# Performance work log

Measured on AMD Instinct MI355X. Metric: run time of the kernel, lower is better.

## Reference

```python
import jax, jax.numpy as jnp
import numpy as np

NUM_CLASSES = 80
CONF_THRESH = 0.05
NMS_THRESH = 0.6
TOPK = 1000
LEVEL_HWS = [40000, 10000, 2500, 640, 160]
CLASS_OFFSET = 2.0  # > max box coordinate so different classes never overlap (class-aware NMS)


def setup_inputs() -> dict:
    key = jax.random.key(0)
    inp = {}
    for i, hw in enumerate(LEVEL_HWS):
        k1, k2, k3, key = jax.random.split(key, 4)
        inp[f"cls_p{i + 3}"] = jax.random.normal(k1, (1, hw, NUM_CLASSES), jnp.float32)
        inp[f"ctn_p{i + 3}"] = jax.random.normal(k2, (1, hw, 1), jnp.float32)
        inp[f"box_p{i + 3}"] = jax.random.uniform(k3, (1, hw, 4), jnp.float32)
    inp["img_size"] = 1600
    return inp


def _level_select(cls_p, ctn_p, box_p):
    # cls_p: [1, HW, C], ctn_p: [1, HW, 1], box_p: [1, HW, 4]
    cls_p, ctn_p, box_p = cls_p[0], ctn_p[0], box_p[0]
    k = min(TOPK, box_p.shape[0])  # matches min(self.topk, box_pred_i.size(0))
    scores = jnp.sqrt(jax.nn.sigmoid(cls_p) * jax.nn.sigmoid(ctn_p)).reshape(-1)  # [HW*C]
    topk_scores, topk_idxs = jax.lax.top_k(scores, k)  # descending, == sort+slice
    valid = topk_scores > CONF_THRESH  # mask instead of dynamic filter (jit-friendly)
    labels = topk_idxs % NUM_CLASSES
    anchor_idxs = topk_idxs // NUM_CLASSES
    return topk_scores * valid, labels, box_p[anchor_idxs], valid


def _pairwise_iou(boxes):
    # boxes: [N, 4] xyxy
    x1, y1, x2, y2 = boxes[:, 0], boxes[:, 1], boxes[:, 2], boxes[:, 3]
    area = jnp.maximum(x2 - x1, 0.0) * jnp.maximum(y2 - y1, 0.0)
    ix1 = jnp.maximum(x1[:, None], x1[None, :])
    iy1 = jnp.maximum(y1[:, None], y1[None, :])
    ix2 = jnp.minimum(x2[:, None], x2[None, :])
    iy2 = jnp.minimum(y2[:, None], y2[None, :])
    inter = jnp.maximum(ix2 - ix1, 0.0) * jnp.maximum(iy2 - iy1, 0.0)
    union = area[:, None] + area[None, :] - inter
    return inter / jnp.maximum(union, 1e-9)


def _greedy_nms(scores, boxes, valid, thresh):
    # exact greedy NMS over a fixed-size candidate set; returns keep mask [N]
    n = scores.shape[0]
    order = jnp.argsort(-scores)
    iou = _pairwise_iou(boxes[order])  # [N, N]
    idx = jnp.arange(n)

    def body(i, keep):
        sup = (iou[i] > thresh) & keep[i] & (idx > i)
        return keep & (~sup)

    keep_o = jax.lax.fori_loop(0, n, body, valid[order])
    return jnp.zeros(n, dtype=bool).at[order].set(keep_o)


def reference(cls_p3, ctn_p3, box_p3, cls_p4, ctn_p4, box_p4,
              cls_p5, ctn_p5, box_p5, cls_p6, ctn_p6, box_p6,
              cls_p7, ctn_p7, box_p7, img_size):
    levels = [(cls_p3, ctn_p3, box_p3), (cls_p4, ctn_p4, box_p4),
              (cls_p5, ctn_p5, box_p5), (cls_p6, ctn_p6, box_p6),
              (cls_p7, ctn_p7, box_p7)]
    parts = [_level_select(c, t, b) for (c, t, b) in levels]
    scores = jnp.concatenate([p[0] for p in parts])   # [3800]
    labels = jnp.concatenate([p[1] for p in parts])   # [3800] int
    bboxes = jnp.concatenate([p[2] for p in parts])   # [3800, 4]
    valid = jnp.concatenate([p[3] for p in parts])    # [3800] bool
    # class-aware multiclass NMS via coordinate offset per class
    boxes_off = bboxes + (labels.astype(bboxes.dtype) * CLASS_OFFSET)[:, None]
    keep = _greedy_nms(jax.lax.stop_gradient(scores),
                       jax.lax.stop_gradient(boxes_off), valid, NMS_THRESH)
    # normalize to [0,1] by image size (square image: W == H == img_size)
    bboxes_n = jnp.clip(bboxes / jnp.float32(img_size), 0.0, 1.0)
    return scores * keep, labels, bboxes_n, keep
```

## Files before the change

kernel.cpp:

```cpp
#include <hip/hip_runtime.h>
#include <math.h>

#pragma clang fp contract(off)

#define NCLS 80
#define NTOT 3800
#define CAND_CAP 4096
#define NMS_CAP 1024
#define BIN_LO 0x3F000000u
#define NB 1024
#define BSHIFT 13
#define QPB 1024
#define NBLK 1044
#define PBUF_CAP 320

__constant__ int d_BSQ[6]  = {0, 782, 978, 1027, 1040, 1044};
__constant__ int d_QL[5]   = {800000, 200000, 50000, 12800, 3200};
__constant__ int d_EL[5]   = {3200000, 800000, 200000, 51200, 12800};
__constant__ float d_PREHI[5] = {0.86f, 0.82f, 0.78f, 0.74f, 0.74f};
__constant__ int d_SEGCAP[5]  = {64, 96, 192, 320, 320};
__constant__ int d_SEGBASE[5] = {0, 50048, 68864, 78272, 82432};
__constant__ int d_KL[5] = {1000,1000,1000,640,160};
__constant__ int d_OB[5] = {0,1000,2000,3000,3640};

struct Params {
  const float *cls0,*cls1,*cls2,*cls3,*cls4;
  const float *ctn0,*ctn1,*ctn2,*ctn3,*ctn4;
  const float *box0,*box1,*box2,*box3,*box4;
  const int* img;
  unsigned short* blockhist;
  unsigned* tot;
  unsigned* blkcnt;
  unsigned long long* pre;
  unsigned long long* ckey;
  unsigned* ccount;
  unsigned* slot_bits;
  unsigned* slot_label;
  float* slot_box;
  float* out;
};

__device__ __forceinline__ float fast_sig(float x) {
  return 1.0f / (1.0f + __expf(-x));
}
__device__ __forceinline__ float fast_score(float c, float t) {
  return sqrtf(fast_sig(c) * fast_sig(t));
}

__device__ __forceinline__ float sigmoid_ref(float x) {
  float e = (float)exp(-(double)x);
  return 1.0f / (1.0f + e);
}
__device__ __forceinline__ float score_ref(float c, float t) {
  return sqrtf(sigmoid_ref(c) * sigmoid_ref(t));
}

__device__ __forceinline__ float iou_ref(float ax1,float ay1,float ax2,float ay2,
                                         float bx1,float by1,float bx2,float by2) {
  float areaA = fmaxf(ax2-ax1,0.0f) * fmaxf(ay2-ay1,0.0f);
  float areaB = fmaxf(bx2-bx1,0.0f) * fmaxf(by2-by1,0.0f);
  float ix1 = fmaxf(ax1,bx1), iy1 = fmaxf(ay1,by1);
  float ix2 = fminf(ax2,bx2), iy2 = fminf(ay2,by2);
  float inter = fmaxf(ix2-ix1,0.0f) * fmaxf(iy2-iy1,0.0f);
  float uni = areaA + areaB - inter;
  return inter / fmaxf(uni, 1e-9f);
}

__device__ __forceinline__ const float* cls_of(const Params& p, int l) {
  return (l==0)?p.cls0:(l==1)?p.cls1:(l==2)?p.cls2:(l==3)?p.cls3:p.cls4;
}
__device__ __forceinline__ const float* ctn_of(const Params& p, int l) {
  return (l==0)?p.ctn0:(l==1)?p.ctn1:(l==2)?p.ctn2:(l==3)?p.ctn3:p.ctn4;
}
__device__ __forceinline__ const float* box_of(const Params& p, int l) {
  return (l==0)?p.box0:(l==1)?p.box1:(l==2)?p.box2:(l==3)?p.box3:p.box4;
}

__global__ __launch_bounds__(256) void k_score(Params p) {
  int b = blockIdx.x, tid = threadIdx.x;
  __shared__ unsigned h[NB];
  __shared__ unsigned long long pbuf[PBUF_CAP];
  __shared__ unsigned pcnt;
  for (int i = tid; i < NB; i += 256) h[i] = 0u;
  if (tid == 0) pcnt = 0u;
  __syncthreads();
  int l = 0;
  while (b >= d_BSQ[l+1]) ++l;
  int cb = b - d_BSQ[l];
  int q0 = cb * QPB;
  int nq = d_QL[l] - q0; if (nq > QPB) nq = QPB;
  const float* cls = cls_of(p, l);
  const float* ctn = ctn_of(p, l);
  float prehi = d_PREHI[l];
  for (int i = tid; i < nq; i += 256) {
    int q = q0 + i;
    float4 c4 = ((const float4*)cls)[q];
    float st = fast_sig(ctn[q / 20]);
    float s[4];
    s[0] = sqrtf(fast_sig(c4.x) * st);
    s[1] = sqrtf(fast_sig(c4.y) * st);
    s[2] = sqrtf(fast_sig(c4.z) * st);
    s[3] = sqrtf(fast_sig(c4.w) * st);
    #pragma unroll
    for (int j = 0; j < 4; ++j) {
      unsigned bits = __float_as_uint(s[j]);
      if (bits >= BIN_LO) atomicAdd(&h[(bits - BIN_LO) >> BSHIFT], 1u);
      if (s[j] >= prehi) {
        unsigned pos = atomicAdd(&pcnt, 1u);
        if (pos < PBUF_CAP)
          pbuf[pos] = ((unsigned long long)bits << 32)
                    | (unsigned long long)(0xFFFFFFFFu - (unsigned)(4*q + j));
      }
    }
  }
  __syncthreads();
  unsigned short* hout = p.blockhist + (size_t)b * NB;
  for (int i = tid; i < NB; i += 256) hout[i] = (unsigned short)h[i];
  int cap = d_SEGCAP[l];
  unsigned n = pcnt;
  if (tid == 0) p.blkcnt[b] = n;
  unsigned nw = n < (unsigned)cap ? n : (unsigned)cap;
  unsigned long long* seg = p.pre + d_SEGBASE[l] + (size_t)cb * cap;
  for (unsigned i = tid; i < nw; i += 256) seg[i] = pbuf[i];
}

__global__ __launch_bounds__(256) void k_reduce(Params p) {
  int l = blockIdx.x >> 4, c = blockIdx.x & 15, tid = threadIdx.x;
  int b0 = d_BSQ[l], rows = d_BSQ[l+1] - b0;
  int bin = c*64 + (tid & 63);
  int rlane = tid >> 6;
  const unsigned short* bh = p.blockhist + (size_t)b0 * NB + bin;
  unsigned a0=0,a1=0,a2=0,a3=0;
  int r = rlane;
  for (; r + 12 < rows; r += 16) {
    a0 += bh[(size_t)r * NB];
    a1 += bh[(size_t)(r+4) * NB];
    a2 += bh[(size_t)(r+8) * NB];
    a3 += bh[(size_t)(r+12) * NB];
  }
  for (; r < rows; r += 4) a0 += bh[(size_t)r * NB];
  __shared__ unsigned red[256];
  red[tid] = a0+a1+a2+a3;
  __syncthreads();
  if (tid < 64)
    p.tot[l*NB + c*64 + tid] = red[tid] + red[tid+64] + red[tid+128] + red[tid+192];
}

__global__ __launch_bounds__(1024) void k_gather(Params p) {
  int l = blockIdx.x, tid = threadIdx.x;
  __shared__ unsigned long long cand[CAND_CAP];
  __shared__ unsigned tot[NB];
  __shared__ unsigned csum[256];
  __shared__ unsigned ccnt;
  __shared__ int bad;
  __shared__ unsigned thr_s;
  if (tid == 0) { ccnt = 0u; bad = 0; }
  if (tid < NB) tot[tid] = p.tot[l*NB + tid];
  __syncthreads();
  if (tid < 256) {
    unsigned s = 0;
    for (int j = 0; j < 4; ++j) s += tot[tid*4 + j];
    csum[tid] = s;
  }
  __syncthreads();
  if (tid == 0) {
    unsigned k = (unsigned)d_KL[l];
    unsigned cum = 0; int chunk = 255;
    for (; chunk > 0; --chunk) {
      if (cum + csum[chunk] >= k) break;
      cum += csum[chunk];
    }
    int binf = 0; int found = 0;
    unsigned c2 = cum;
    for (int i = 3; i >= 0; --i) {
      int bin = chunk*4 + i;
      c2 += tot[bin];
      if (c2 >= k) { binf = bin; found = 1; break; }
    }
    unsigned t = BIN_LO;
    if (found && binf > 0) t = BIN_LO + ((unsigned)(binf - 1) << BSHIFT);
    thr_s = t;
  }
  __syncthreads();
  unsigned thr = thr_s;
  int b0 = d_BSQ[l], nseg = d_BSQ[l+1] - b0, cap = d_SEGCAP[l];
  for (int s = tid; s < nseg; s += 1024)
    if (p.blkcnt[b0 + s] > (unsigned)cap) bad = 1;
  __syncthreads();
  const float* cls = cls_of(p, l);
  const float* ctn = ctn_of(p, l);
  bool fastok = (!bad) && (thr >= __float_as_uint(d_PREHI[l]));
  if (fastok) {
    int total = nseg * cap;
    const unsigned long long* base = p.pre + d_SEGBASE[l];
    for (int i = tid; i < total; i += 1024) {
      int s = i / cap, j = i - s*cap;
      if (j < (int)p.blkcnt[b0 + s]) {
        unsigned long long kk = base[(size_t)s*cap + j];
        if ((unsigned)(kk >> 32) >= thr) {
          unsigned pos = atomicAdd(&ccnt, 1u);
          if (pos < CAND_CAP) cand[pos] = kk;
        }
      }
    }
  } else {
    int ne = d_EL[l];
    for (int e = tid; e < ne; e += 1024) {
      float s = fast_score(cls[e], ctn[e / NCLS]);
      unsigned bits = __float_as_uint(s);
      if (bits >= thr) {
        unsigned pos = atomicAdd(&ccnt, 1u);
        if (pos < CAND_CAP)
          cand[pos] = ((unsigned long long)bits << 32)
                    | (unsigned long long)(0xFFFFFFFFu - (unsigned)e);
      }
    }
  }
  __syncthreads();
  int m = (ccnt < CAND_CAP) ? (int)ccnt : CAND_CAP;
  unsigned long long* ck = p.ckey + (size_t)l * CAND_CAP;
  for (int i = tid; i < m; i += 1024) {
    unsigned fi = 0xFFFFFFFFu - (unsigned)(cand[i] & 0xFFFFFFFFu);
    float ex = score_ref(cls[fi], ctn[fi / NCLS]);
    ck[i] = ((unsigned long long)__float_as_uint(ex) << 32)
          | (unsigned long long)(0xFFFFFFFFu - fi);
  }
  if (tid == 0) p.ccount[l] = (unsigned)m;
  int kL = d_KL[l], obase = d_OB[l];
  for (int r = m + tid; r < kL; r += 1024) {
    int g = obase + r;
    p.out[NTOT + g] = 0.0f;
    for (int j = 0; j < 4; ++j) { p.out[2*NTOT + g*4 + j] = 0.0f; p.slot_box[g*4+j] = 0.0f; }
    p.slot_bits[g] = 0u; p.slot_label[g] = 0u;
  }
}

__global__ __launch_bounds__(64) void k_rank(Params p) {
  int bx = blockIdx.x;
  int l = bx >> 6, slice = bx & 63;
  int tid = threadIdx.x;
  __shared__ unsigned long long key[CAND_CAP];
  int m = (int)p.ccount[l];
  int i0 = slice * 64;
  if (i0 >= m) return;
  const unsigned long long* ck = p.ckey + (size_t)l * CAND_CAP;
  for (int j = tid; j < m; j += 64) key[j] = ck[j];
  __syncthreads();
  int i = i0 + tid;
  if (i >= m) return;
  unsigned long long mine = key[i];
  int rank = 0;
  int mm = m & ~7;
  #pragma unroll 1
  for (int j = 0; j < mm; j += 8) {
    rank += (key[j  ] > mine) + (key[j+1] > mine) + (key[j+2] > mine) + (key[j+3] > mine)
          + (key[j+4] > mine) + (key[j+5] > mine) + (key[j+6] > mine) + (key[j+7] > mine);
  }
  for (int j = mm; j < m; ++j) rank += (key[j] > mine) ? 1 : 0;
  if (rank >= d_KL[l]) return;
  int g = d_OB[l] + rank;
  unsigned bits = (unsigned)(mine >> 32);
  unsigned fi = 0xFFFFFFFFu - (unsigned)(mine & 0xFFFFFFFFu);
  unsigned lab = fi % NCLS;
  unsigned a = fi / NCLS;
  float img = (float)(*p.img);
  float4 b4 = ((const float4*)box_of(p, l))[a];
  float4 nb;
  nb.x = fminf(fmaxf(b4.x / img, 0.0f), 1.0f);
  nb.y = fminf(fmaxf(b4.y / img, 0.0f), 1.0f);
  nb.z = fminf(fmaxf(b4.z / img, 0.0f), 1.0f);
  nb.w = fminf(fmaxf(b4.w / img, 0.0f), 1.0f);
  p.out[NTOT + g] = (float)lab;
  ((float4*)(p.out + 2*NTOT))[g] = nb;
  ((float4*)p.slot_box)[g] = b4;
  p.slot_bits[g] = bits;
  p.slot_label[g] = lab;
}

__global__ __launch_bounds__(64) void k_nms(Params p) {
  int c = blockIdx.x, tid = threadIdx.x;
  __shared__ unsigned mcnt;
  __shared__ unsigned long long key[NMS_CAP];
  __shared__ unsigned long long skey[NMS_CAP];
  __shared__ float bx[NMS_CAP*4];
  __shared__ int keep[NMS_CAP];
  if (tid == 0) mcnt = 0u;
  __syncthreads();
  for (int g = tid; g < NTOT; g += 64) {
    if (p.slot_label[g] == (unsigned)c) {
      unsigned pos = atomicAdd(&mcnt, 1u);
      if (pos < NMS_CAP)
        key[pos] = ((unsigned long long)p.slot_bits[g] << 32)
                 | (unsigned long long)(0xFFFFFFFFu - (unsigned)g);
    }
  }
  __syncthreads();
  int m = (mcnt < NMS_CAP) ? (int)mcnt : NMS_CAP;
  if (m == 0) return;
  for (int i = tid; i < m; i += 64) {
    unsigned long long mine = key[i];
    int rank = 0;
    for (int j = 0; j < m; ++j) rank += (key[j] > mine) ? 1 : 0;
    skey[rank] = mine;
  }
  __syncthreads();
  float off = 2.0f * (float)c;
  for (int j = tid; j < m; j += 64) {
    unsigned long long kk = skey[j];
    unsigned g = 0xFFFFFFFFu - (unsigned)(kk & 0xFFFFFFFFu);
    for (int q = 0; q < 4; ++q) bx[j*4+q] = p.slot_box[g*4+q] + off;
    float s = __uint_as_float((unsigned)(kk >> 32));
    keep[j] = (s > 0.05f) ? 1 : 0;
  }
  __syncthreads();
  for (int i = 0; i + 1 < m; ++i) {
    if (keep[i]) {
      float ax1 = bx[i*4+0], ay1 = bx[i*4+1], ax2 = bx[i*4+2], ay2 = bx[i*4+3];
      for (int j = i + 1 + tid; j < m; j += 64) {
        if (keep[j]) {
          if (iou_ref(ax1,ay1,ax2,ay2, bx[j*4+0],bx[j*4+1],bx[j*4+2],bx[j*4+3]) > 0.6f)
            keep[j] = 0;
        }
      }
    }
    __syncthreads();
  }
  for (int j = tid; j < m; j += 64) {
    unsigned long long kk = skey[j];
    unsigned g = 0xFFFFFFFFu - (unsigned)(kk & 0xFFFFFFFFu);
    float s = __uint_as_float((unsigned)(kk >> 32));
    int kp = keep[j];
    p.out[g] = kp ? s : 0.0f;
    p.out[6*NTOT + g] = kp ? 1.0f : 0.0f;
  }
}

extern "C" void kernel_launch(void* const* d_in, const int* in_sizes, int n_in,
                              void* d_out, int out_size, void* d_ws, size_t ws_size,
                              hipStream_t stream) {
  Params p;
  p.cls0 = (const float*)d_in[0];  p.ctn0 = (const float*)d_in[1];  p.box0 = (const float*)d_in[2];
  p.cls1 = (const float*)d_in[3];  p.ctn1 = (const float*)d_in[4];  p.box1 = (const float*)d_in[5];
  p.cls2 = (const float*)d_in[6];  p.ctn2 = (const float*)d_in[7];  p.box2 = (const float*)d_in[8];
  p.cls3 = (const float*)d_in[9];  p.ctn3 = (const float*)d_in[10]; p.box3 = (const float*)d_in[11];
  p.cls4 = (const float*)d_in[12]; p.ctn4 = (const float*)d_in[13]; p.box4 = (const float*)d_in[14];
  p.img  = (const int*)d_in[15];

  char* w = (char*)d_ws;
  p.pre = (unsigned long long*)w;   w += (size_t)83712 * 8;
  p.blockhist = (unsigned short*)w; w += (size_t)NBLK*NB*2;
  p.tot  = (unsigned*)w;            w += (size_t)5*NB*4;
  p.blkcnt = (unsigned*)w;          w += (size_t)NBLK*4 + 64;
  p.ckey = (unsigned long long*)w;  w += (size_t)5*CAND_CAP*8;
  p.ccount = (unsigned*)w;          w += 32;
  p.slot_bits  = (unsigned*)w;      w += NTOT*4;
  p.slot_label = (unsigned*)w;      w += NTOT*4;
  p.slot_box   = (float*)w;         w += NTOT*16;
  p.out = (float*)d_out;

  hipLaunchKernelGGL(k_score,  dim3(NBLK),  dim3(256),  0, stream, p);
  hipLaunchKernelGGL(k_reduce, dim3(80),    dim3(256),  0, stream, p);
  hipLaunchKernelGGL(k_gather, dim3(5),     dim3(1024), 0, stream, p);
  hipLaunchKernelGGL(k_rank,   dim3(5*64),  dim3(64),   0, stream, p);
  hipLaunchKernelGGL(k_nms,    dim3(80),    dim3(64),   0, stream, p);
}
```

Baseline: 218.5 us.

## Restructure pipeline: atomic histograms, split gather, per-class buckets, wave-level NMS

Per-block histograms are now folded straight into a global histogram with atomics, which removes the separate reduce kernel and the large short-histogram buffer. The gather stage runs on 40 blocks instead of 5, finds the threshold with a parallel suffix scan and computes exact scores inline. The rank kernel appends each kept candidate into a per-class bucket, so NMS no longer scans all 3800 slots for every class. Classes with at most 64 boxes run a single-wavefront NMS using ballot and shuffle instead of shared memory and barriers. The cost is one extra zeroing kernel plus more global atomics, whose order can vary between runs.

```diff
diff --git a/kernel.cpp b/kernel.cpp
--- a/kernel.cpp
+++ b/kernel.cpp
@@ -2,24 +2,26 @@
 #include <math.h>
 
 #pragma clang fp contract(off)
+
+typedef unsigned long long ull;
 
 #define NCLS 80
 #define NTOT 3800
 #define CAND_CAP 4096
 #define NMS_CAP 1024
+#define CLS_CAP 128
 #define BIN_LO 0x3F000000u
 #define NB 1024
 #define BSHIFT 13
 #define QPB 1024
 #define NBLK 1044
-#define PBUF_CAP 320
+#define SEGCAP 320
+#define ZWORDS 6496
 
 __constant__ int d_BSQ[6]  = {0, 782, 978, 1027, 1040, 1044};
 __constant__ int d_QL[5]   = {800000, 200000, 50000, 12800, 3200};
 __constant__ int d_EL[5]   = {3200000, 800000, 200000, 51200, 12800};
 __constant__ float d_PREHI[5] = {0.86f, 0.82f, 0.78f, 0.74f, 0.74f};
-__constant__ int d_SEGCAP[5]  = {64, 96, 192, 320, 320};
-__constant__ int d_SEGBASE[5] = {0, 50048, 68864, 78272, 82432};
 __constant__ int d_KL[5] = {1000,1000,1000,640,160};
 __constant__ int d_OB[5] = {0,1000,2000,3000,3640};
 
@@ -28,12 +30,14 @@
   const float *ctn0,*ctn1,*ctn2,*ctn3,*ctn4;
   const float *box0,*box1,*box2,*box3,*box4;
   const int* img;
-  unsigned short* blockhist;
+  ull* pre;
   unsigned* tot;
+  unsigned* ccount;
+  unsigned* clscnt;
+  unsigned* lvlbad;
   unsigned* blkcnt;
-  unsigned long long* pre;
-  unsigned long long* ckey;
-  unsigned* ccount;
+  ull* ckey;
+  ull* clskey;
   unsigned* slot_bits;
   unsigned* slot_label;
   float* slot_box;
@@ -46,7 +50,6 @@
 __device__ __forceinline__ float fast_score(float c, float t) {
   return sqrtf(fast_sig(c) * fast_sig(t));
 }
-
 __device__ __forceinline__ float sigmoid_ref(float x) {
   float e = (float)exp(-(double)x);
   return 1.0f / (1.0f + e);
@@ -54,7 +57,6 @@
 __device__ __forceinline__ float score_ref(float c, float t) {
   return sqrtf(sigmoid_ref(c) * sigmoid_ref(t));
 }
-
 __device__ __forceinline__ float iou_ref(float ax1,float ay1,float ax2,float ay2,
                                          float bx1,float by1,float bx2,float by2) {
   float areaA = fmaxf(ax2-ax1,0.0f) * fmaxf(ay2-ay1,0.0f);
@@ -65,7 +67,6 @@
   float uni = areaA + areaB - inter;
   return inter / fmaxf(uni, 1e-9f);
 }
-
 __device__ __forceinline__ const float* cls_of(const Params& p, int l) {
   return (l==0)?p.cls0:(l==1)?p.cls1:(l==2)?p.cls2:(l==3)?p.cls3:p.cls4;
 }
@@ -74,12 +75,16 @@
 }
 __device__ __forceinline__ const float* box_of(const Params& p, int l) {
   return (l==0)?p.box0:(l==1)?p.box1:(l==2)?p.box2:(l==3)?p.box3:p.box4;
+}
+
+__global__ __launch_bounds__(256) void k_zero(unsigned* z) {
+  for (int i = blockIdx.x*256 + threadIdx.x; i < ZWORDS; i += 256) z[i] = 0u;
 }
 
 __global__ __launch_bounds__(256) void k_score(Params p) {
   int b = blockIdx.x, tid = threadIdx.x;
   __shared__ unsigned h[NB];
-  __shared__ unsigned long long pbuf[PBUF_CAP];
+  __shared__ ull pbuf[SEGCAP];
   __shared__ unsigned pcnt;
   for (int i = tid; i < NB; i += 256) h[i] = 0u;
   if (tid == 0) pcnt = 0u;
@@ -107,131 +112,116 @@
       if (bits >= BIN_LO) atomicAdd(&h[(bits - BIN_LO) >> BSHIFT], 1u);
       if (s[j] >= prehi) {
         unsigned pos = atomicAdd(&pcnt, 1u);
-        if (pos < PBUF_CAP)
-          pbuf[pos] = ((unsigned long long)bits << 32)
-                    | (unsigned long long)(0xFFFFFFFFu - (unsigned)(4*q + j));
-      }
-    }
-  }
-  __syncthreads();
-  unsigned short* hout = p.blockhist + (size_t)b * NB;
-  for (int i = tid; i < NB; i += 256) hout[i] = (unsigned short)h[i];
-  int cap = d_SEGCAP[l];
+        if (pos < SEGCAP)
+          pbuf[pos] = ((ull)bits << 32) | (ull)(0xFFFFFFFFu - (unsigned)(4*q + j));
+      }
+    }
+  }
+  __syncthreads();
+  unsigned* tl = p.tot + l*NB;
+  for (int i = tid; i < NB; i += 256) {
+    unsigned v = h[i];
+    if (v) atomicAdd(&tl[i], v);
+  }
   unsigned n = pcnt;
-  if (tid == 0) p.blkcnt[b] = n;
-  unsigned nw = n < (unsigned)cap ? n : (unsigned)cap;
-  unsigned long long* seg = p.pre + d_SEGBASE[l] + (size_t)cb * cap;
+  if (tid == 0) {
+    p.blkcnt[b] = n;
+    if (n > SEGCAP) p.lvlbad[l] = 1u;
+  }
+  unsigned nw = n < SEGCAP ? n : SEGCAP;
+  ull* seg = p.pre + (size_t)b * SEGCAP;
   for (unsigned i = tid; i < nw; i += 256) seg[i] = pbuf[i];
 }
 
-__global__ __launch_bounds__(256) void k_reduce(Params p) {
-  int l = blockIdx.x >> 4, c = blockIdx.x & 15, tid = threadIdx.x;
-  int b0 = d_BSQ[l], rows = d_BSQ[l+1] - b0;
-  int bin = c*64 + (tid & 63);
-  int rlane = tid >> 6;
-  const unsigned short* bh = p.blockhist + (size_t)b0 * NB + bin;
-  unsigned a0=0,a1=0,a2=0,a3=0;
-  int r = rlane;
-  for (; r + 12 < rows; r += 16) {
-    a0 += bh[(size_t)r * NB];
-    a1 += bh[(size_t)(r+4) * NB];
-    a2 += bh[(size_t)(r+8) * NB];
-    a3 += bh[(size_t)(r+12) * NB];
-  }
-  for (; r < rows; r += 4) a0 += bh[(size_t)r * NB];
-  __shared__ unsigned red[256];
-  red[tid] = a0+a1+a2+a3;
-  __syncthreads();
-  if (tid < 64)
-    p.tot[l*NB + c*64 + tid] = red[tid] + red[tid+64] + red[tid+128] + red[tid+192];
-}
-
-__global__ __launch_bounds__(1024) void k_gather(Params p) {
-  int l = blockIdx.x, tid = threadIdx.x;
-  __shared__ unsigned long long cand[CAND_CAP];
-  __shared__ unsigned tot[NB];
-  __shared__ unsigned csum[256];
-  __shared__ unsigned ccnt;
-  __shared__ int bad;
-  __shared__ unsigned thr_s;
-  if (tid == 0) { ccnt = 0u; bad = 0; }
-  if (tid < NB) tot[tid] = p.tot[l*NB + tid];
-  __syncthreads();
-  if (tid < 256) {
-    unsigned s = 0;
-    for (int j = 0; j < 4; ++j) s += tot[tid*4 + j];
-    csum[tid] = s;
-  }
-  __syncthreads();
-  if (tid == 0) {
-    unsigned k = (unsigned)d_KL[l];
-    unsigned cum = 0; int chunk = 255;
-    for (; chunk > 0; --chunk) {
-      if (cum + csum[chunk] >= k) break;
-      cum += csum[chunk];
-    }
-    int binf = 0; int found = 0;
-    unsigned c2 = cum;
-    for (int i = 3; i >= 0; --i) {
-      int bin = chunk*4 + i;
-      c2 += tot[bin];
-      if (c2 >= k) { binf = bin; found = 1; break; }
-    }
-    unsigned t = BIN_LO;
-    if (found && binf > 0) t = BIN_LO + ((unsigned)(binf - 1) << BSHIFT);
-    thr_s = t;
-  }
-  __syncthreads();
-  unsigned thr = thr_s;
-  int b0 = d_BSQ[l], nseg = d_BSQ[l+1] - b0, cap = d_SEGCAP[l];
-  for (int s = tid; s < nseg; s += 1024)
-    if (p.blkcnt[b0 + s] > (unsigned)cap) bad = 1;
-  __syncthreads();
+__global__ __launch_bounds__(256) void k_gather(Params p) {
+  int bx = blockIdx.x;
+  int l = bx >> 3, slice = bx & 7;
+  int tid = threadIdx.x;
+  __shared__ unsigned sfx[NB];
+  __shared__ ull cbuf[CAND_CAP];
+  __shared__ unsigned pcnt;
+  __shared__ unsigned thr_sh;
+  __shared__ unsigned base_sh;
+  if (tid == 0) { pcnt = 0u; thr_sh = BIN_LO; }
+  for (int j = tid; j < NB; j += 256) sfx[j] = p.tot[l*NB + j];
+  __syncthreads();
+  for (int off = 1; off < NB; off <<= 1) {
+    unsigned v[4];
+    #pragma unroll
+    for (int j = 0; j < 4; ++j) {
+      int idx = tid + j*256;
+      unsigned add = (idx + off < NB) ? sfx[idx + off] : 0u;
+      v[j] = sfx[idx] + add;
+    }
+    __syncthreads();
+    #pragma unroll
+    for (int j = 0; j < 4; ++j) sfx[tid + j*256] = v[j];
+    __syncthreads();
+  }
+  unsigned k = (unsigned)d_KL[l];
+  #pragma unroll
+  for (int j = 0; j < 4; ++j) {
+    int b = tid + j*256;
+    unsigned s0 = sfx[b];
+    unsigned s1 = (b + 1 < NB) ? sfx[b+1] : 0u;
+    if (s0 >= k && (b == NB-1 || s1 < k)) {
+      thr_sh = (b > 0) ? (BIN_LO + ((unsigned)(b-1) << BSHIFT)) : BIN_LO;
+    }
+  }
+  __syncthreads();
+  unsigned thr = thr_sh;
   const float* cls = cls_of(p, l);
   const float* ctn = ctn_of(p, l);
-  bool fastok = (!bad) && (thr >= __float_as_uint(d_PREHI[l]));
-  if (fastok) {
-    int total = nseg * cap;
-    const unsigned long long* base = p.pre + d_SEGBASE[l];
-    for (int i = tid; i < total; i += 1024) {
-      int s = i / cap, j = i - s*cap;
-      if (j < (int)p.blkcnt[b0 + s]) {
-        unsigned long long kk = base[(size_t)s*cap + j];
+  bool fallback = (p.lvlbad[l] != 0u) || (thr < __float_as_uint(d_PREHI[l]));
+  if (!fallback) {
+    int s0b = d_BSQ[l], nseg = d_BSQ[l+1] - s0b;
+    int chunk = (nseg + 7) >> 3;
+    int sA = slice * chunk, sB = sA + chunk;
+    if (sA > nseg) sA = nseg;
+    if (sB > nseg) sB = nseg;
+    int total = (sB - sA) * SEGCAP;
+    const ull* base = p.pre + (size_t)(s0b + sA) * SEGCAP;
+    const unsigned* bc = p.blkcnt + s0b + sA;
+    for (int i = tid; i < total; i += 256) {
+      int s = i / SEGCAP;
+      int j = i - s * SEGCAP;
+      unsigned cnt = bc[s]; if (cnt > SEGCAP) cnt = SEGCAP;
+      if (j < (int)cnt) {
+        ull kk = base[(size_t)s * SEGCAP + j];
         if ((unsigned)(kk >> 32) >= thr) {
-          unsigned pos = atomicAdd(&ccnt, 1u);
-          if (pos < CAND_CAP) cand[pos] = kk;
+          unsigned fi = 0xFFFFFFFFu - (unsigned)kk;
+          float ex = score_ref(cls[fi], ctn[fi / NCLS]);
+          unsigned pos = atomicAdd(&pcnt, 1u);
+          if (pos < CAND_CAP)
+            cbuf[pos] = ((ull)__float_as_uint(ex) << 32) | (ull)(0xFFFFFFFFu - fi);
         }
       }
     }
   } else {
     int ne = d_EL[l];
-    for (int e = tid; e < ne; e += 1024) {
+    int chunk = (ne + 7) >> 3;
+    int eA = slice * chunk, eB = eA + chunk;
+    if (eA > ne) eA = ne;
+    if (eB > ne) eB = ne;
+    for (int e = eA + tid; e < eB; e += 256) {
       float s = fast_score(cls[e], ctn[e / NCLS]);
-      unsigned bits = __float_as_uint(s);
-      if (bits >= thr) {
-        unsigned pos = atomicAdd(&ccnt, 1u);
+      if (__float_as_uint(s) >= thr) {
+        float ex = score_ref(cls[e], ctn[e / NCLS]);
+        unsigned pos = atomicAdd(&pcnt, 1u);
         if (pos < CAND_CAP)
-          cand[pos] = ((unsigned long long)bits << 32)
-                    | (unsigned long long)(0xFFFFFFFFu - (unsigned)e);
-      }
-    }
-  }
-  __syncthreads();
-  int m = (ccnt < CAND_CAP) ? (int)ccnt : CAND_CAP;
-  unsigned long long* ck = p.ckey + (size_t)l * CAND_CAP;
-  for (int i = tid; i < m; i += 1024) {
-    unsigned fi = 0xFFFFFFFFu - (unsigned)(cand[i] & 0xFFFFFFFFu);
-    float ex = score_ref(cls[fi], ctn[fi / NCLS]);
-    ck[i] = ((unsigned long long)__float_as_uint(ex) << 32)
-          | (unsigned long long)(0xFFFFFFFFu - fi);
-  }
-  if (tid == 0) p.ccount[l] = (unsigned)m;
-  int kL = d_KL[l], obase = d_OB[l];
-  for (int r = m + tid; r < kL; r += 1024) {
-    int g = obase + r;
-    p.out[NTOT + g] = 0.0f;
-    for (int j = 0; j < 4; ++j) { p.out[2*NTOT + g*4 + j] = 0.0f; p.slot_box[g*4+j] = 0.0f; }
-    p.slot_bits[g] = 0u; p.slot_label[g] = 0u;
+          cbuf[pos] = ((ull)__float_as_uint(ex) << 32) | (ull)(0xFFFFFFFFu - (unsigned)e);
+      }
+    }
+  }
+  __syncthreads();
+  unsigned n = pcnt; if (n > CAND_CAP) n = CAND_CAP;
+  if (tid == 0) base_sh = atomicAdd(&p.ccount[l*16], n);
+  __syncthreads();
+  unsigned bp = base_sh;
+  ull* ck = p.ckey + (size_t)l * CAND_CAP;
+  for (unsigned i = tid; i < n; i += 256) {
+    unsigned d = bp + i;
+    if (d < CAND_CAP) ck[d] = cbuf[i];
   }
 }
 
@@ -239,16 +229,41 @@
   int bx = blockIdx.x;
   int l = bx >> 6, slice = bx & 63;
   int tid = threadIdx.x;
-  __shared__ unsigned long long key[CAND_CAP];
-  int m = (int)p.ccount[l];
+  int m = (int)p.ccount[l*16]; if (m > CAND_CAP) m = CAND_CAP;
+  int kL = d_KL[l], obase = d_OB[l];
   int i0 = slice * 64;
-  if (i0 >= m) return;
-  const unsigned long long* ck = p.ckey + (size_t)l * CAND_CAP;
+  int i = i0 + tid;
+  if (i0 >= m) {
+    if (i >= m && i < kL) {
+      int g = obase + i;
+      p.out[g] = 0.0f;
+      p.out[NTOT + g] = 0.0f;
+      ((float4*)(p.out + 2*NTOT))[g] = make_float4(0,0,0,0);
+      p.out[6*NTOT + g] = 0.0f;
+      ((float4*)p.slot_box)[g] = make_float4(0,0,0,0);
+      p.slot_bits[g] = 0u;
+      p.slot_label[g] = 0xFFFFFFFFu;
+    }
+    return;
+  }
+  __shared__ ull key[CAND_CAP];
+  const ull* ck = p.ckey + (size_t)l * CAND_CAP;
   for (int j = tid; j < m; j += 64) key[j] = ck[j];
   __syncthreads();
-  int i = i0 + tid;
-  if (i >= m) return;
-  unsigned long long mine = key[i];
+  if (i >= m) {
+    if (i < kL) {
+      int g = obase + i;
+      p.out[g] = 0.0f;
+      p.out[NTOT + g] = 0.0f;
+      ((float4*)(p.out + 2*NTOT))[g] = make_float4(0,0,0,0);
+      p.out[6*NTOT + g] = 0.0f;
+      ((float4*)p.slot_box)[g] = make_float4(0,0,0,0);
+      p.slot_bits[g] = 0u;
+      p.slot_label[g] = 0xFFFFFFFFu;
+    }
+    return;
+  }
+  ull mine = key[i];
   int rank = 0;
   int mm = m & ~7;
   #pragma unroll 1
@@ -257,8 +272,8 @@
           + (key[j+4] > mine) + (key[j+5] > mine) + (key[j+6] > mine) + (key[j+7] > mine);
   }
   for (int j = mm; j < m; ++j) rank += (key[j] > mine) ? 1 : 0;
-  if (rank >= d_KL[l]) return;
-  int g = d_OB[l] + rank;
+  if (rank >= kL) return;
+  int g = obase + rank;
   unsigned bits = (unsigned)(mine >> 32);
   unsigned fi = 0xFFFFFFFFu - (unsigned)(mine & 0xFFFFFFFFu);
   unsigned lab = fi % NCLS;
@@ -275,58 +290,106 @@
   ((float4*)p.slot_box)[g] = b4;
   p.slot_bits[g] = bits;
   p.slot_label[g] = lab;
+  unsigned pos = atomicAdd(&p.clscnt[lab*16], 1u);
+  if (pos < CLS_CAP)
+    p.clskey[lab*CLS_CAP + pos] = ((ull)bits << 32) | (ull)(0xFFFFFFFFu - (unsigned)g);
 }
 
 __global__ __launch_bounds__(64) void k_nms(Params p) {
-  int c = blockIdx.x, tid = threadIdx.x;
-  __shared__ unsigned mcnt;
-  __shared__ unsigned long long key[NMS_CAP];
-  __shared__ unsigned long long skey[NMS_CAP];
-  __shared__ float bx[NMS_CAP*4];
+  int c = blockIdx.x, lane = threadIdx.x;
+  int mc = (int)p.clscnt[c*16];
+  if (mc == 0) return;
+  if (mc <= 64) {
+    ull kk = (lane < mc) ? p.clskey[c*CLS_CAP + lane] : 0ULL;
+    int rank = 0;
+    #pragma unroll 1
+    for (int j = 0; j < 64; ++j) {
+      ull kj = __shfl(kk, j);
+      rank += (j < mc && kj > kk) ? 1 : 0;
+    }
+    __shared__ ull wkey[64];
+    if (lane < mc) wkey[rank] = kk;
+    __syncthreads();
+    ull sk = (lane < mc) ? wkey[lane] : 0ULL;
+    unsigned g = 0xFFFFFFFFu - (unsigned)(sk & 0xFFFFFFFFu);
+    float s = __uint_as_float((unsigned)(sk >> 32));
+    float off = 2.0f * (float)c;
+    float x1=0,y1=0,x2=0,y2=0;
+    if (lane < mc) {
+      float4 b4 = ((const float4*)p.slot_box)[g];
+      x1 = b4.x + off; y1 = b4.y + off; x2 = b4.z + off; y2 = b4.w + off;
+    }
+    ull keepm = __ballot(lane < mc && s > 0.05f);
+    for (int i = 0; i + 1 < mc; ++i) {
+      if ((keepm >> i) & 1ULL) {
+        float ax1 = __shfl(x1, i), ay1 = __shfl(y1, i);
+        float ax2 = __shfl(x2, i), ay2 = __shfl(y2, i);
+        bool kept = (keepm >> lane) & 1ULL;
+        bool sup = kept && (lane > i) && (lane < mc) &&
+                   (iou_ref(ax1,ay1,ax2,ay2, x1,y1,x2,y2) > 0.6f);
+        keepm &= ~__ballot(sup);
+      }
+    }
+    if (lane < mc) {
+      int kp = (int)((keepm >> lane) & 1ULL);
+      p.out[g] = kp ? s : 0.0f;
+      p.out[6*NTOT + g] = kp ? 1.0f : 0.0f;
+    }
+    return;
+  }
+  __shared__ ull key[NMS_CAP];
+  __shared__ ull skey[NMS_CAP];
+  __shared__ float bxs[NMS_CAP*4];
   __shared__ int keep[NMS_CAP];
-  if (tid == 0) mcnt = 0u;
-  __syncthreads();
-  for (int g = tid; g < NTOT; g += 64) {
-    if (p.slot_label[g] == (unsigned)c) {
-      unsigned pos = atomicAdd(&mcnt, 1u);
-      if (pos < NMS_CAP)
-        key[pos] = ((unsigned long long)p.slot_bits[g] << 32)
-                 | (unsigned long long)(0xFFFFFFFFu - (unsigned)g);
-    }
-  }
-  __syncthreads();
-  int m = (mcnt < NMS_CAP) ? (int)mcnt : NMS_CAP;
-  if (m == 0) return;
-  for (int i = tid; i < m; i += 64) {
-    unsigned long long mine = key[i];
+  __shared__ unsigned mcnt_s;
+  int m;
+  if (mc <= CLS_CAP) {
+    for (int j = lane; j < mc; j += 64) key[j] = p.clskey[c*CLS_CAP + j];
+    m = mc;
+    __syncthreads();
+  } else {
+    if (lane == 0) mcnt_s = 0u;
+    __syncthreads();
+    for (int g = lane; g < NTOT; g += 64) {
+      if (p.slot_label[g] == (unsigned)c) {
+        unsigned pos = atomicAdd(&mcnt_s, 1u);
+        if (pos < NMS_CAP)
+          key[pos] = ((ull)p.slot_bits[g] << 32) | (ull)(0xFFFFFFFFu - (unsigned)g);
+      }
+    }
+    __syncthreads();
+    m = (mcnt_s < NMS_CAP) ? (int)mcnt_s : NMS_CAP;
+  }
+  for (int i = lane; i < m; i += 64) {
+    ull mine = key[i];
     int rank = 0;
     for (int j = 0; j < m; ++j) rank += (key[j] > mine) ? 1 : 0;
     skey[rank] = mine;
   }
   __syncthreads();
   float off = 2.0f * (float)c;
-  for (int j = tid; j < m; j += 64) {
-    unsigned long long kk = skey[j];
+  for (int j = lane; j < m; j += 64) {
+    ull kk = skey[j];
     unsigned g = 0xFFFFFFFFu - (unsigned)(kk & 0xFFFFFFFFu);
-    for (int q = 0; q < 4; ++q) bx[j*4+q] = p.slot_box[g*4+q] + off;
+    for (int q = 0; q < 4; ++q) bxs[j*4+q] = p.slot_box[g*4+q] + off;
     float s = __uint_as_float((unsigned)(kk >> 32));
     keep[j] = (s > 0.05f) ? 1 : 0;
   }
   __syncthreads();
   for (int i = 0; i + 1 < m; ++i) {
     if (keep[i]) {
-      float ax1 = bx[i*4+0], ay1 = bx[i*4+1], ax2 = bx[i*4+2], ay2 = bx[i*4+3];
-      for (int j = i + 1 + tid; j < m; j += 64) {
+      float ax1 = bxs[i*4+0], ay1 = bxs[i*4+1], ax2 = bxs[i*4+2], ay2 = bxs[i*4+3];
+      for (int j = i + 1 + lane; j < m; j += 64) {
         if (keep[j]) {
-          if (iou_ref(ax1,ay1,ax2,ay2, bx[j*4+0],bx[j*4+1],bx[j*4+2],bx[j*4+3]) > 0.6f)
+          if (iou_ref(ax1,ay1,ax2,ay2, bxs[j*4+0],bxs[j*4+1],bxs[j*4+2],bxs[j*4+3]) > 0.6f)
             keep[j] = 0;
         }
       }
     }
     __syncthreads();
   }
-  for (int j = tid; j < m; j += 64) {
-    unsigned long long kk = skey[j];
+  for (int j = lane; j < m; j += 64) {
+    ull kk = skey[j];
     unsigned g = 0xFFFFFFFFu - (unsigned)(kk & 0xFFFFFFFFu);
     float s = __uint_as_float((unsigned)(kk >> 32));
     int kp = keep[j];
@@ -347,20 +410,24 @@
   p.img  = (const int*)d_in[15];
 
   char* w = (char*)d_ws;
-  p.pre = (unsigned long long*)w;   w += (size_t)83712 * 8;
-  p.blockhist = (unsigned short*)w; w += (size_t)NBLK*NB*2;
-  p.tot  = (unsigned*)w;            w += (size_t)5*NB*4;
-  p.blkcnt = (unsigned*)w;          w += (size_t)NBLK*4 + 64;
-  p.ckey = (unsigned long long*)w;  w += (size_t)5*CAND_CAP*8;
-  p.ccount = (unsigned*)w;          w += 32;
-  p.slot_bits  = (unsigned*)w;      w += NTOT*4;
-  p.slot_label = (unsigned*)w;      w += NTOT*4;
-  p.slot_box   = (float*)w;         w += NTOT*16;
+  p.pre = (ull*)w;            w += (size_t)NBLK*SEGCAP*8;
+  unsigned* zbase = (unsigned*)w;
+  p.tot    = zbase;
+  p.ccount = zbase + 5120;
+  p.clscnt = zbase + 5120 + 80;
+  p.lvlbad = zbase + 5120 + 80 + 1280;
+  w += (size_t)ZWORDS*4;
+  p.blkcnt = (unsigned*)w;    w += (size_t)NBLK*4 + 64;
+  p.ckey = (ull*)w;           w += (size_t)5*CAND_CAP*8;
+  p.clskey = (ull*)w;         w += (size_t)NCLS*CLS_CAP*8;
+  p.slot_bits  = (unsigned*)w; w += NTOT*4;
+  p.slot_label = (unsigned*)w; w += NTOT*4;
+  p.slot_box   = (float*)w;    w += NTOT*16;
   p.out = (float*)d_out;
 
-  hipLaunchKernelGGL(k_score,  dim3(NBLK),  dim3(256),  0, stream, p);
-  hipLaunchKernelGGL(k_reduce, dim3(80),    dim3(256),  0, stream, p);
-  hipLaunchKernelGGL(k_gather, dim3(5),     dim3(1024), 0, stream, p);
-  hipLaunchKernelGGL(k_rank,   dim3(5*64),  dim3(64),   0, stream, p);
-  hipLaunchKernelGGL(k_nms,    dim3(80),    dim3(64),   0, stream, p);
-}
+  hipLaunchKernelGGL(k_zero,   dim3(1),     dim3(256), 0, stream, zbase);
+  hipLaunchKernelGGL(k_score,  dim3(NBLK),  dim3(256), 0, stream, p);
+  hipLaunchKernelGGL(k_gather, dim3(40),    dim3(256), 0, stream, p);
+  hipLaunchKernelGGL(k_rank,   dim3(5*64),  dim3(64),  0, stream, p);
+  hipLaunchKernelGGL(k_nms,    dim3(80),    dim3(64),  0, stream, p);
+}
```

After: 209.5 us. 1.04x faster.
